# Performance work log

Hardware: AMD Instinct MI355X
Metric: run time of the kernel (lower is better)

Reference implementation:

```python
import jax, jax.numpy as jnp
import numpy as np

N_NODES = 100000
N_EDGES = 1600000
NFEAT, NHID, NCLASS = 256, 256, 64
NLAYERS = 4


def _gcn_norm(edge_index, n_nodes):
    # PyG GCNConv default: add self-loops, symmetric normalization
    src, dst = edge_index[0], edge_index[1]
    loop = jnp.arange(n_nodes, dtype=edge_index.dtype)
    src = jnp.concatenate([src, loop])
    dst = jnp.concatenate([dst, loop])
    deg = jax.ops.segment_sum(jnp.ones_like(dst, dtype=jnp.float32), dst,
                              num_segments=n_nodes)
    dinv = jnp.where(deg > 0, jax.lax.rsqrt(deg), 0.0)
    norm = dinv[src] * dinv[dst]  # [E+N]
    return src, dst, norm


def _gcn_layer(X, W, b, src, dst, norm, n_nodes):
    H = X @ W                      # [N, out]
    msg = H[src] * norm[:, None]   # [E+N, out] gather + scale
    out = jax.ops.segment_sum(msg, dst, num_segments=n_nodes)
    return out + b


def setup_inputs() -> dict:
    key = jax.random.key(0)
    ks = jax.random.split(key, 8)
    x = jax.random.normal(ks[0], (N_NODES, NFEAT), dtype=jnp.float32)
    edge_index = jax.random.randint(ks[1], (2, N_EDGES), 0, N_NODES, dtype=jnp.int32)
    def glorot(k, fan_in, fan_out):
        s = jnp.sqrt(6.0 / (fan_in + fan_out))
        return jax.random.uniform(k, (fan_in, fan_out), jnp.float32, -s, s)
    return {
        "x": x,
        "W_enc": glorot(ks[2], NFEAT, NHID),
        "b_enc": jnp.zeros((NHID,), jnp.float32),
        "W_conv": glorot(ks[3], NHID, NHID),
        "b_conv": jnp.zeros((NHID,), jnp.float32),
        "W_dec": glorot(ks[4], NHID, NCLASS),
        "b_dec": jnp.zeros((NCLASS,), jnp.float32),
        "edge_index": edge_index,
    }


def reference(x, W_enc, b_enc, W_conv, b_conv, W_dec, b_dec, edge_index):
    n_nodes = x.shape[0]
    src, dst, norm = _gcn_norm(edge_index, n_nodes)
    # dropout probs are 0 (drop_in=drop=0) -> identity
    X = jax.nn.relu(_gcn_layer(x, W_enc, b_enc, src, dst, norm, n_nodes))
    for _ in range(NLAYERS):
        X = jax.nn.relu(_gcn_layer(X, W_conv, b_conv, src, dst, norm, n_nodes))
    X = jax.nn.relu(_gcn_layer(X, W_dec, b_dec, src, dst, norm, n_nodes))
    return X
```

## Files before the change

kernel.cpp:

```cpp
#include <hip/hip_runtime.h>

#define N_NODES 100000
#define N_EDGES 1600000
#define MPAD    100096
#define NB_SCAN ((N_NODES + 255) / 256)

using short8 = __attribute__((ext_vector_type(8))) short;
using f32x4  = __attribute__((ext_vector_type(4))) float;

__device__ inline unsigned short f2bf(float f) {
    unsigned u = __float_as_uint(f);
    unsigned r = (u + 0x7fffu + ((u >> 16) & 1u)) >> 16;
    return (unsigned short)r;
}
__device__ inline float bf2f(unsigned short h) {
    return __uint_as_float(((unsigned)h) << 16);
}


__global__ __launch_bounds__(256) void k_init(int* __restrict__ indeg,
                                              int* __restrict__ cursor, int n) {
    int i = blockIdx.x * blockDim.x + threadIdx.x;
    if (i < n) { indeg[i] = 0; cursor[i] = 0; }
}

__global__ __launch_bounds__(256) void k_indeg(const int* __restrict__ dst,
                                               int* __restrict__ indeg, int e) {
    int i = blockIdx.x * blockDim.x + threadIdx.x;
    if (i < e) atomicAdd(&indeg[dst[i]], 1);
}

__global__ __launch_bounds__(256) void k_scan_blocks(const int* __restrict__ indeg,
                                                     int* __restrict__ blksum, int n) {
    int i = blockIdx.x * 256 + threadIdx.x;
    int v = (i < n) ? indeg[i] : 0;
#pragma unroll
    for (int o = 32; o > 0; o >>= 1) v += __shfl_down(v, o, 64);
    __shared__ int ws[4];
    if ((threadIdx.x & 63) == 0) ws[threadIdx.x >> 6] = v;
    __syncthreads();
    if (threadIdx.x == 0) blksum[blockIdx.x] = ws[0] + ws[1] + ws[2] + ws[3];
}

__global__ __launch_bounds__(512) void k_scan_top(const int* __restrict__ blksum,
                                                  int* __restrict__ blkpref,
                                                  int* __restrict__ offsets, int nb, int n) {
    __shared__ int s[512];
    int t = threadIdx.x;
    int v = (t < nb) ? blksum[t] : 0;
    s[t] = v;
    __syncthreads();
    for (int o = 1; o < 512; o <<= 1) {
        int u = (t >= o) ? s[t - o] : 0;
        __syncthreads();
        s[t] += u;
        __syncthreads();
    }
    if (t < nb) blkpref[t] = (t == 0) ? 0 : s[t - 1];
    if (t == nb - 1) offsets[n] = s[t];
}

__global__ __launch_bounds__(256) void k_scan_final(const int* __restrict__ indeg,
                                                    const int* __restrict__ blkpref,
                                                    int* __restrict__ offsets,
                                                    float* __restrict__ dinv, int n) {
    __shared__ int s[256];
    int t = threadIdx.x;
    int i = blockIdx.x * 256 + t;
    int v = (i < n) ? indeg[i] : 0;
    s[t] = v;
    __syncthreads();
    for (int o = 1; o < 256; o <<= 1) {
        int u = (t >= o) ? s[t - o] : 0;
        __syncthreads();
        s[t] += u;
        __syncthreads();
    }
    if (i < n) {
        offsets[i] = blkpref[blockIdx.x] + s[t] - v;
        dinv[i] = rsqrtf((float)(v + 1));
    }
}

__global__ __launch_bounds__(256) void k_scatter(const int* __restrict__ src,
                                                 const int* __restrict__ dst,
                                                 const float* __restrict__ dinv,
                                                 const int* __restrict__ offsets,
                                                 int* __restrict__ cursor,
                                                 int* __restrict__ csr_src,
                                                 float* __restrict__ csr_norm, int e) {
    int i = blockIdx.x * blockDim.x + threadIdx.x;
    if (i < e) {
        int d = dst[i], s = src[i];
        int pos = offsets[d] + atomicAdd(&cursor[d], 1);
        csr_src[pos] = s;
        csr_norm[pos] = dinv[s] * dinv[d];
    }
}


__global__ __launch_bounds__(256) void k_cvt_x(const float* __restrict__ x,
                                               unsigned short* __restrict__ xb) {
    int i = blockIdx.x * blockDim.x + threadIdx.x;
    int row = i >> 6;
    ushort4 o;
    if (row < N_NODES) {
        float4 v = *(const float4*)(x + (size_t)i * 4);
        o.x = f2bf(v.x); o.y = f2bf(v.y); o.z = f2bf(v.z); o.w = f2bf(v.w);
    } else {
        o.x = o.y = o.z = o.w = 0;
    }
    *(ushort4*)(xb + (size_t)i * 4) = o;
}

__global__ __launch_bounds__(256) void k_prep_w(const float* __restrict__ W,
                                                unsigned short* __restrict__ Wt, int N) {
    int i = blockIdx.x * blockDim.x + threadIdx.x;
    if (i < 256 * N) {
        int r = i / N, c = i - r * N;
        Wt[(size_t)c * 256 + r] = f2bf(W[i]);
    }
}


template <int BN>
__global__ __launch_bounds__(256) void k_mfma_gemm(const unsigned short* __restrict__ A,
                                                   const unsigned short* __restrict__ Bt,
                                                   unsigned short* __restrict__ C,
                                                   int Ntot) {
    constexpr int K = 256, BK = 64;
    constexpr int NFR = BN / 32;
    __shared__ char ldsA[128 * 128];
    __shared__ char ldsB[BN * 128];
    const int tid  = threadIdx.x;
    const int lane = tid & 63;
    const int wid  = tid >> 6;
    const int wr   = wid >> 1, wc = wid & 1;
    const int row0 = blockIdx.x * 128;
    const int col0 = blockIdx.y * BN;
    const int l15  = lane & 15, lhi = lane >> 4;

    f32x4 acc[4][NFR];
#pragma unroll
    for (int m = 0; m < 4; ++m)
#pragma unroll
        for (int n = 0; n < NFR; ++n) acc[m][n] = {0.f, 0.f, 0.f, 0.f};

    for (int k0 = 0; k0 < K; k0 += BK) {
#pragma unroll
        for (int j = 0; j < 4; ++j) {
            int ci = j * 256 + tid;
            int r = ci >> 3;
            int cb = (ci & 7) ^ (r & 7);
            const char* src = (const char*)(A + (size_t)(row0 + r) * K + k0) + cb * 16;
            __builtin_amdgcn_global_load_lds((const __attribute__((address_space(1))) void*)src,
                                             (__attribute__((address_space(3))) void*)(ldsA + ci * 16),
                                             16, 0, 0);
        }
#pragma unroll
        for (int j = 0; j < BN / 32; ++j) {
            int ci = j * 256 + tid;
            int r = ci >> 3;
            int cb = (ci & 7) ^ (r & 7);
            const char* src = (const char*)(Bt + (size_t)(col0 + r) * K + k0) + cb * 16;
            __builtin_amdgcn_global_load_lds((const __attribute__((address_space(1))) void*)src,
                                             (__attribute__((address_space(3))) void*)(ldsB + ci * 16),
                                             16, 0, 0);
        }
        __syncthreads();
#pragma unroll
        for (int kk = 0; kk < 2; ++kk) {
            short8 af[4], bfr[NFR];
            int cb = kk * 4 + lhi;
#pragma unroll
            for (int m = 0; m < 4; ++m) {
                int r = wr * 64 + m * 16 + l15;
                af[m] = *(const short8*)(ldsA + r * 128 + ((cb ^ (r & 7)) << 4));
            }
#pragma unroll
            for (int n = 0; n < NFR; ++n) {
                int r = wc * (NFR * 16) + n * 16 + l15;
                bfr[n] = *(const short8*)(ldsB + r * 128 + ((cb ^ (r & 7)) << 4));
            }
#pragma unroll
            for (int m = 0; m < 4; ++m)
#pragma unroll
                for (int n = 0; n < NFR; ++n)
                    acc[m][n] = __builtin_amdgcn_mfma_f32_16x16x32_bf16(af[m], bfr[n],
                                                                        acc[m][n], 0, 0, 0);
        }
        __syncthreads();
    }
#pragma unroll
    for (int m = 0; m < 4; ++m)
#pragma unroll
        for (int n = 0; n < NFR; ++n) {
            int col = col0 + wc * (NFR * 16) + n * 16 + l15;
            int rbase = row0 + wr * 64 + m * 16 + lhi * 4;
#pragma unroll
            for (int q = 0; q < 4; ++q)
                C[(size_t)(rbase + q) * Ntot + col] = f2bf(acc[m][n][q]);
        }
}


template <int VEC, typename OUT>
__global__ __launch_bounds__(256) void k_aggregate(const unsigned short* __restrict__ H,
                                                   const int* __restrict__ offsets,
                                                   const int* __restrict__ csr_src,
                                                   const float* __restrict__ csr_norm,
                                                   const float* __restrict__ dinv,
                                                   const float* __restrict__ bias,
                                                   OUT* __restrict__ out, int n) {
    constexpr int F = 64 * VEC;
    const int wid = (blockIdx.x * blockDim.x + threadIdx.x) >> 6;
    const int lane = threadIdx.x & 63;
    if (wid >= n) return;

    float acc[VEC];
#pragma unroll
    for (int v = 0; v < VEC; ++v) acc[v] = 0.f;

    const int beg = offsets[wid], end = offsets[wid + 1];
    int e = beg;
    for (; e + 3 < end; e += 4) {
        int s0 = csr_src[e], s1 = csr_src[e + 1], s2 = csr_src[e + 2], s3 = csr_src[e + 3];
        float n0 = csr_norm[e], n1 = csr_norm[e + 1], n2 = csr_norm[e + 2], n3 = csr_norm[e + 3];
        if (VEC == 4) {
            ushort4 v0 = *(const ushort4*)(H + (size_t)s0 * F + (lane << 2));
            ushort4 v1 = *(const ushort4*)(H + (size_t)s1 * F + (lane << 2));
            ushort4 v2 = *(const ushort4*)(H + (size_t)s2 * F + (lane << 2));
            ushort4 v3 = *(const ushort4*)(H + (size_t)s3 * F + (lane << 2));
            acc[0] += bf2f(v0.x) * n0 + bf2f(v1.x) * n1 + bf2f(v2.x) * n2 + bf2f(v3.x) * n3;
            acc[1] += bf2f(v0.y) * n0 + bf2f(v1.y) * n1 + bf2f(v2.y) * n2 + bf2f(v3.y) * n3;
            acc[2] += bf2f(v0.z) * n0 + bf2f(v1.z) * n1 + bf2f(v2.z) * n2 + bf2f(v3.z) * n3;
            acc[3] += bf2f(v0.w) * n0 + bf2f(v1.w) * n1 + bf2f(v2.w) * n2 + bf2f(v3.w) * n3;
        } else {
            acc[0] += bf2f(H[(size_t)s0 * F + lane]) * n0 + bf2f(H[(size_t)s1 * F + lane]) * n1
                    + bf2f(H[(size_t)s2 * F + lane]) * n2 + bf2f(H[(size_t)s3 * F + lane]) * n3;
        }
    }
    for (; e < end; ++e) {
        int s = csr_src[e];
        float nrm = csr_norm[e];
        if (VEC == 4) {
            ushort4 v = *(const ushort4*)(H + (size_t)s * F + (lane << 2));
            acc[0] += bf2f(v.x) * nrm; acc[1] += bf2f(v.y) * nrm;
            acc[2] += bf2f(v.z) * nrm; acc[3] += bf2f(v.w) * nrm;
        } else {
            acc[0] += bf2f(H[(size_t)s * F + lane]) * nrm;
        }
    }
    float dv = dinv[wid];
    float sw = dv * dv;
    if (VEC == 4) {
        ushort4 v = *(const ushort4*)(H + (size_t)wid * F + (lane << 2));
        float4 b = *(const float4*)(bias + (lane << 2));
        float r0 = fmaxf(acc[0] + bf2f(v.x) * sw + b.x, 0.f);
        float r1 = fmaxf(acc[1] + bf2f(v.y) * sw + b.y, 0.f);
        float r2 = fmaxf(acc[2] + bf2f(v.z) * sw + b.z, 0.f);
        float r3 = fmaxf(acc[3] + bf2f(v.w) * sw + b.w, 0.f);
        if constexpr (sizeof(OUT) == 2) {
            ushort4 o; o.x = f2bf(r0); o.y = f2bf(r1); o.z = f2bf(r2); o.w = f2bf(r3);
            *(ushort4*)((unsigned short*)out + (size_t)wid * F + (lane << 2)) = o;
        } else {
            *(float4*)((float*)out + (size_t)wid * F + (lane << 2)) = make_float4(r0, r1, r2, r3);
        }
    } else {
        float r = fmaxf(acc[0] + bf2f(H[(size_t)wid * F + lane]) * sw + bias[lane], 0.f);
        if constexpr (sizeof(OUT) == 2)
            ((unsigned short*)out)[(size_t)wid * F + lane] = f2bf(r);
        else
            ((float*)out)[(size_t)wid * F + lane] = r;
    }
}


extern "C" void kernel_launch(void* const* d_in, const int* in_sizes, int n_in,
                              void* d_out, int out_size, void* d_ws, size_t ws_size,
                              hipStream_t stream) {
    const float* x      = (const float*)d_in[0];
    const float* W_enc  = (const float*)d_in[1];
    const float* b_enc  = (const float*)d_in[2];
    const float* W_conv = (const float*)d_in[3];
    const float* b_conv = (const float*)d_in[4];
    const float* W_dec  = (const float*)d_in[5];
    const float* b_dec  = (const float*)d_in[6];
    const int*   ei     = (const int*)d_in[7];

    const int N = N_NODES;
    const int E = N_EDGES;
    const int* src = ei;
    const int* dst = ei + E;

    size_t off = 0;
    auto carve = [&](size_t bytes) -> void* {
        void* p = (char*)d_ws + off;
        off = (off + bytes + 255) & ~(size_t)255;
        return p;
    };
    unsigned short* Xb      = (unsigned short*)carve((size_t)MPAD * 256 * 2);
    unsigned short* Hb      = (unsigned short*)carve((size_t)MPAD * 256 * 2);
    unsigned short* Wt_enc  = (unsigned short*)carve((size_t)256 * 256 * 2);
    unsigned short* Wt_conv = (unsigned short*)carve((size_t)256 * 256 * 2);
    unsigned short* Wt_dec  = (unsigned short*)carve((size_t)64 * 256 * 2);
    int*            indeg   = (int*)carve((size_t)N * sizeof(int));
    int*            cursor  = (int*)carve((size_t)N * sizeof(int));
    float*          dinv    = (float*)carve((size_t)N * sizeof(float));
    int*            offsets = (int*)carve((size_t)(N + 1) * sizeof(int));
    int*            csr_src = (int*)carve((size_t)E * sizeof(int));
    float*          csr_nrm = (float*)carve((size_t)E * sizeof(float));
    int*            blksum  = (int*)carve((size_t)NB_SCAN * sizeof(int));
    int*            blkpref = (int*)carve((size_t)NB_SCAN * sizeof(int));
    (void)ws_size;

    k_cvt_x<<<MPAD / 4, 256, 0, stream>>>(x, Xb);
    k_prep_w<<<(256 * 256 + 255) / 256, 256, 0, stream>>>(W_enc, Wt_enc, 256);
    k_prep_w<<<(256 * 256 + 255) / 256, 256, 0, stream>>>(W_conv, Wt_conv, 256);
    k_prep_w<<<(256 * 64 + 255) / 256, 256, 0, stream>>>(W_dec, Wt_dec, 64);
    k_init<<<(N + 255) / 256, 256, 0, stream>>>(indeg, cursor, N);
    k_indeg<<<(E + 255) / 256, 256, 0, stream>>>(dst, indeg, E);
    k_scan_blocks<<<NB_SCAN, 256, 0, stream>>>(indeg, blksum, N);
    k_scan_top<<<1, 512, 0, stream>>>(blksum, blkpref, offsets, NB_SCAN, N);
    k_scan_final<<<NB_SCAN, 256, 0, stream>>>(indeg, blkpref, offsets, dinv, N);
    k_scatter<<<(E + 255) / 256, 256, 0, stream>>>(src, dst, dinv, offsets, cursor,
                                                   csr_src, csr_nrm, E);

    dim3 gconv(MPAD / 128, 2);
    dim3 gdec(MPAD / 128, 1);
    const int agg_blocks = (N * 64 + 255) / 256;

    k_mfma_gemm<128><<<gconv, 256, 0, stream>>>(Xb, Wt_enc, Hb, 256);
    k_aggregate<4, unsigned short><<<agg_blocks, 256, 0, stream>>>(Hb, offsets, csr_src,
                                                                   csr_nrm, dinv, b_enc, Xb, N);
    for (int l = 0; l < 4; ++l) {
        k_mfma_gemm<128><<<gconv, 256, 0, stream>>>(Xb, Wt_conv, Hb, 256);
        k_aggregate<4, unsigned short><<<agg_blocks, 256, 0, stream>>>(Hb, offsets, csr_src,
                                                                       csr_nrm, dinv, b_conv, Xb, N);
    }
    k_mfma_gemm<64><<<gdec, 256, 0, stream>>>(Xb, Wt_dec, Hb, 64);
    k_aggregate<1, float><<<agg_blocks, 256, 0, stream>>>(Hb, offsets, csr_src,
                                                          csr_nrm, dinv, b_dec,
                                                          (float*)d_out, N);
}
```

Baseline: 1.003 ms.

## Split wavefront into half/quarter groups gathering different edges with wider loads

The aggregation kernels are rewritten so each wavefront processes two edges at a time (256-wide) or four edges at a time (64-wide). Each lane group gathers a full row with 16-byte or 8-byte vector loads. The partial sums are combined with cross-lane shuffles, and the self-loop term is folded into the tail iteration. This is meant to raise gather width and memory-level parallelism per lane and reduce per-edge instruction overhead. In exchange it adds shuffle reductions, and half or more of the lanes sit idle at the store. It also switches to 32-bit offsets and scalarises the node index with readfirstlane.

```diff
diff --git a/kernel.cpp b/kernel.cpp
--- a/kernel.cpp
+++ b/kernel.cpp
@@ -5,8 +5,9 @@
 #define MPAD    100096
 #define NB_SCAN ((N_NODES + 255) / 256)
 
-using short8 = __attribute__((ext_vector_type(8))) short;
-using f32x4  = __attribute__((ext_vector_type(4))) float;
+using short8  = __attribute__((ext_vector_type(8))) short;
+using ushort8 = __attribute__((ext_vector_type(8))) unsigned short;
+using f32x4   = __attribute__((ext_vector_type(4))) float;
 
 __device__ inline unsigned short f2bf(float f) {
     unsigned u = __float_as_uint(f);
@@ -204,74 +205,124 @@
 }
 
 
-template <int VEC, typename OUT>
-__global__ __launch_bounds__(256) void k_aggregate(const unsigned short* __restrict__ H,
-                                                   const int* __restrict__ offsets,
-                                                   const int* __restrict__ csr_src,
-                                                   const float* __restrict__ csr_norm,
-                                                   const float* __restrict__ dinv,
-                                                   const float* __restrict__ bias,
-                                                   OUT* __restrict__ out, int n) {
-    constexpr int F = 64 * VEC;
-    const int wid = (blockIdx.x * blockDim.x + threadIdx.x) >> 6;
+__global__ __launch_bounds__(256) void k_agg256(const unsigned short* __restrict__ H,
+                                                const int* __restrict__ offsets,
+                                                const int* __restrict__ csr_src,
+                                                const float* __restrict__ csr_norm,
+                                                const float* __restrict__ dinv,
+                                                const float* __restrict__ bias,
+                                                unsigned short* __restrict__ out, int n) {
+    const int wid = __builtin_amdgcn_readfirstlane((blockIdx.x * blockDim.x + threadIdx.x) >> 6);
+    if (wid >= n) return;
     const int lane = threadIdx.x & 63;
-    if (wid >= n) return;
-
-    float acc[VEC];
-#pragma unroll
-    for (int v = 0; v < VEC; ++v) acc[v] = 0.f;
-
+    const int half = lane >> 5;
+    const unsigned coff = (unsigned)(lane & 31) * 16u;
+
+    float acc[8] = {};
     const int beg = offsets[wid], end = offsets[wid + 1];
     int e = beg;
+
+    auto do_pair = [&](int ea) {
+        int s0 = csr_src[ea], s1 = csr_src[ea + 1];
+        float n0 = csr_norm[ea], n1 = csr_norm[ea + 1];
+        unsigned off = (unsigned)(half ? s1 : s0) * 512u + coff;
+        float nrm = half ? n1 : n0;
+        ushort8 v = *(const ushort8*)((const char*)H + off);
+#pragma unroll
+        for (int j = 0; j < 8; ++j) acc[j] = fmaf(bf2f(v[j]), nrm, acc[j]);
+    };
+
+    for (; e + 3 < end; e += 4) { do_pair(e); do_pair(e + 2); }
+    for (; e + 1 < end; e += 2) { do_pair(e); }
+
+    {
+        float dv = dinv[wid];
+        float sw = dv * dv;
+        int  has_tail = (e < end);
+        int   sA = has_tail ? csr_src[e]  : wid;
+        float nA = has_tail ? csr_norm[e] : sw;
+        float nB = has_tail ? sw : 0.f;
+        unsigned off = (unsigned)(half ? wid : sA) * 512u + coff;
+        float nrm = half ? nB : nA;
+        ushort8 v = *(const ushort8*)((const char*)H + off);
+#pragma unroll
+        for (int j = 0; j < 8; ++j) acc[j] = fmaf(bf2f(v[j]), nrm, acc[j]);
+    }
+
+#pragma unroll
+    for (int j = 0; j < 8; ++j) acc[j] += __shfl_xor(acc[j], 32);
+
+    if (half == 0) {
+        const float* bp = bias + (lane & 31) * 8;
+        float4 b0 = *(const float4*)bp;
+        float4 b1 = *(const float4*)(bp + 4);
+        ushort8 o;
+        o[0] = f2bf(fmaxf(acc[0] + b0.x, 0.f));
+        o[1] = f2bf(fmaxf(acc[1] + b0.y, 0.f));
+        o[2] = f2bf(fmaxf(acc[2] + b0.z, 0.f));
+        o[3] = f2bf(fmaxf(acc[3] + b0.w, 0.f));
+        o[4] = f2bf(fmaxf(acc[4] + b1.x, 0.f));
+        o[5] = f2bf(fmaxf(acc[5] + b1.y, 0.f));
+        o[6] = f2bf(fmaxf(acc[6] + b1.z, 0.f));
+        o[7] = f2bf(fmaxf(acc[7] + b1.w, 0.f));
+        *(ushort8*)((char*)out + (unsigned)wid * 512u + coff) = o;
+    }
+}
+
+
+__global__ __launch_bounds__(256) void k_agg64(const unsigned short* __restrict__ H,
+                                               const int* __restrict__ offsets,
+                                               const int* __restrict__ csr_src,
+                                               const float* __restrict__ csr_norm,
+                                               const float* __restrict__ dinv,
+                                               const float* __restrict__ bias,
+                                               float* __restrict__ out, int n) {
+    const int wid = __builtin_amdgcn_readfirstlane((blockIdx.x * blockDim.x + threadIdx.x) >> 6);
+    if (wid >= n) return;
+    const int lane = threadIdx.x & 63;
+    const int q = lane >> 4;
+    const unsigned coff = (unsigned)(lane & 15) * 8u;
+
+    float acc[4] = {};
+    const int beg = offsets[wid], end = offsets[wid + 1];
+    int e = beg;
+
     for (; e + 3 < end; e += 4) {
         int s0 = csr_src[e], s1 = csr_src[e + 1], s2 = csr_src[e + 2], s3 = csr_src[e + 3];
         float n0 = csr_norm[e], n1 = csr_norm[e + 1], n2 = csr_norm[e + 2], n3 = csr_norm[e + 3];
-        if (VEC == 4) {
-            ushort4 v0 = *(const ushort4*)(H + (size_t)s0 * F + (lane << 2));
-            ushort4 v1 = *(const ushort4*)(H + (size_t)s1 * F + (lane << 2));
-            ushort4 v2 = *(const ushort4*)(H + (size_t)s2 * F + (lane << 2));
-            ushort4 v3 = *(const ushort4*)(H + (size_t)s3 * F + (lane << 2));
-            acc[0] += bf2f(v0.x) * n0 + bf2f(v1.x) * n1 + bf2f(v2.x) * n2 + bf2f(v3.x) * n3;
-            acc[1] += bf2f(v0.y) * n0 + bf2f(v1.y) * n1 + bf2f(v2.y) * n2 + bf2f(v3.y) * n3;
-            acc[2] += bf2f(v0.z) * n0 + bf2f(v1.z) * n1 + bf2f(v2.z) * n2 + bf2f(v3.z) * n3;
-            acc[3] += bf2f(v0.w) * n0 + bf2f(v1.w) * n1 + bf2f(v2.w) * n2 + bf2f(v3.w) * n3;
-        } else {
-            acc[0] += bf2f(H[(size_t)s0 * F + lane]) * n0 + bf2f(H[(size_t)s1 * F + lane]) * n1
-                    + bf2f(H[(size_t)s2 * F + lane]) * n2 + bf2f(H[(size_t)s3 * F + lane]) * n3;
-        }
-    }
-    for (; e < end; ++e) {
-        int s = csr_src[e];
-        float nrm = csr_norm[e];
-        if (VEC == 4) {
-            ushort4 v = *(const ushort4*)(H + (size_t)s * F + (lane << 2));
-            acc[0] += bf2f(v.x) * nrm; acc[1] += bf2f(v.y) * nrm;
-            acc[2] += bf2f(v.z) * nrm; acc[3] += bf2f(v.w) * nrm;
-        } else {
-            acc[0] += bf2f(H[(size_t)s * F + lane]) * nrm;
-        }
-    }
-    float dv = dinv[wid];
-    float sw = dv * dv;
-    if (VEC == 4) {
-        ushort4 v = *(const ushort4*)(H + (size_t)wid * F + (lane << 2));
-        float4 b = *(const float4*)(bias + (lane << 2));
-        float r0 = fmaxf(acc[0] + bf2f(v.x) * sw + b.x, 0.f);
-        float r1 = fmaxf(acc[1] + bf2f(v.y) * sw + b.y, 0.f);
-        float r2 = fmaxf(acc[2] + bf2f(v.z) * sw + b.z, 0.f);
-        float r3 = fmaxf(acc[3] + bf2f(v.w) * sw + b.w, 0.f);
-        if constexpr (sizeof(OUT) == 2) {
-            ushort4 o; o.x = f2bf(r0); o.y = f2bf(r1); o.z = f2bf(r2); o.w = f2bf(r3);
-            *(ushort4*)((unsigned short*)out + (size_t)wid * F + (lane << 2)) = o;
-        } else {
-            *(float4*)((float*)out + (size_t)wid * F + (lane << 2)) = make_float4(r0, r1, r2, r3);
-        }
-    } else {
-        float r = fmaxf(acc[0] + bf2f(H[(size_t)wid * F + lane]) * sw + bias[lane], 0.f);
-        if constexpr (sizeof(OUT) == 2)
-            ((unsigned short*)out)[(size_t)wid * F + lane] = f2bf(r);
-        else
-            ((float*)out)[(size_t)wid * F + lane] = r;
+        int srow = s0; float nrm = n0;
+        if (q == 1) { srow = s1; nrm = n1; }
+        else if (q == 2) { srow = s2; nrm = n2; }
+        else if (q == 3) { srow = s3; nrm = n3; }
+        ushort4 v = *(const ushort4*)((const char*)H + (unsigned)srow * 128u + coff);
+        acc[0] = fmaf(bf2f(v.x), nrm, acc[0]);
+        acc[1] = fmaf(bf2f(v.y), nrm, acc[1]);
+        acc[2] = fmaf(bf2f(v.z), nrm, acc[2]);
+        acc[3] = fmaf(bf2f(v.w), nrm, acc[3]);
+    }
+    {
+        float dv = dinv[wid];
+        float sw = dv * dv;
+        int r = end - e;
+        int srow = wid; float nrm = 0.f;
+        if (q < r) { srow = csr_src[e + q]; nrm = csr_norm[e + q]; }
+        else if (q == r) { srow = wid; nrm = sw; }
+        ushort4 v = *(const ushort4*)((const char*)H + (unsigned)srow * 128u + coff);
+        acc[0] = fmaf(bf2f(v.x), nrm, acc[0]);
+        acc[1] = fmaf(bf2f(v.y), nrm, acc[1]);
+        acc[2] = fmaf(bf2f(v.z), nrm, acc[2]);
+        acc[3] = fmaf(bf2f(v.w), nrm, acc[3]);
+    }
+#pragma unroll
+    for (int j = 0; j < 4; ++j) {
+        acc[j] += __shfl_xor(acc[j], 16);
+        acc[j] += __shfl_xor(acc[j], 32);
+    }
+    if (q == 0) {
+        float4 b = *(const float4*)(bias + (lane & 15) * 4);
+        float4 o = make_float4(fmaxf(acc[0] + b.x, 0.f), fmaxf(acc[1] + b.y, 0.f),
+                               fmaxf(acc[2] + b.z, 0.f), fmaxf(acc[3] + b.w, 0.f));
+        *(float4*)((char*)out + (size_t)wid * 256u + coff * 2u) = o;
     }
 }
 
@@ -328,18 +379,15 @@
 
     dim3 gconv(MPAD / 128, 2);
     dim3 gdec(MPAD / 128, 1);
-    const int agg_blocks = (N * 64 + 255) / 256;
+    const int agg_blocks = (N + 3) / 4;
 
     k_mfma_gemm<128><<<gconv, 256, 0, stream>>>(Xb, Wt_enc, Hb, 256);
-    k_aggregate<4, unsigned short><<<agg_blocks, 256, 0, stream>>>(Hb, offsets, csr_src,
-                                                                   csr_nrm, dinv, b_enc, Xb, N);
+    k_agg256<<<agg_blocks, 256, 0, stream>>>(Hb, offsets, csr_src, csr_nrm, dinv, b_enc, Xb, N);
     for (int l = 0; l < 4; ++l) {
         k_mfma_gemm<128><<<gconv, 256, 0, stream>>>(Xb, Wt_conv, Hb, 256);
-        k_aggregate<4, unsigned short><<<agg_blocks, 256, 0, stream>>>(Hb, offsets, csr_src,
-                                                                       csr_nrm, dinv, b_conv, Xb, N);
+        k_agg256<<<agg_blocks, 256, 0, stream>>>(Hb, offsets, csr_src, csr_nrm, dinv, b_conv, Xb, N);
     }
     k_mfma_gemm<64><<<gdec, 256, 0, stream>>>(Xb, Wt_dec, Hb, 64);
-    k_aggregate<1, float><<<agg_blocks, 256, 0, stream>>>(Hb, offsets, csr_src,
-                                                          csr_nrm, dinv, b_dec,
-                                                          (float*)d_out, N);
-}
+    k_agg64<<<agg_blocks, 256, 0, stream>>>(Hb, offsets, csr_src, csr_nrm, dinv, b_dec,
+                                            (float*)d_out, N);
+}
```

After: 1.033 ms. 1.03x slower.
